# Performance work log

Measured on AMD Instinct MI355X. Metric: run time of the kernel, lower is better.

The kernel has to match this reference:

```python
import jax, jax.numpy as jnp
import numpy as np

VOCAB = 32000
HIDDEN = 1024
BATCH = 32
SEQ = 128


def setup_inputs() -> dict:
    key = jax.random.key(0)
    ks = jax.random.split(key, 8)
    p = lambda k, shape: (jax.random.normal(k, shape, dtype=jnp.float32) * 0.01)
    return {
        "x": jax.random.randint(ks[0], (BATCH, SEQ), 0, VOCAB, dtype=jnp.int64),
        "state": jnp.zeros((BATCH, HIDDEN), dtype=jnp.float32),
        "W_xr": p(ks[1], (VOCAB, HIDDEN)),
        "W_hr": p(ks[2], (HIDDEN, HIDDEN)),
        "b_r": jnp.zeros((HIDDEN,), dtype=jnp.float32),
        "W_xz": p(ks[3], (VOCAB, HIDDEN)),
        "W_hz": p(ks[4], (HIDDEN, HIDDEN)),
        "b_z": jnp.zeros((HIDDEN,), dtype=jnp.float32),
        "W_xh": p(ks[5], (VOCAB, HIDDEN)),
        "W_hh": p(ks[6], (HIDDEN, HIDDEN)),
        "b_h": jnp.zeros((HIDDEN,), dtype=jnp.float32),
        "W_ho": p(ks[7], (HIDDEN, VOCAB)),
        "b_o": jnp.zeros((VOCAB,), dtype=jnp.float32),
    }


def reference(x, state, W_xr, W_hr, b_r, W_xz, W_hz, b_z, W_xh, W_hh, b_h, W_ho, b_o):
    # x: (B, T) int tokens -> transpose to (T, B) like torch `x.T`.
    # one_hot(tok) @ W_x* is mathematically an embedding row gather: W_x*[tok].
    tokens = x.T  # (T, B)

    def step(h, tok):
        xr = W_xr[tok]  # (B, H)
        xz = W_xz[tok]
        xh = W_xh[tok]
        r = jax.nn.sigmoid(xr + h @ W_hr + b_r)
        z = jax.nn.sigmoid(xz + h @ W_hz + b_z)
        cand = jnp.tanh(xh + (r * h) @ W_hh + b_h)
        h_new = z * h + (1.0 - z) * cand
        out = h_new @ W_ho + b_o  # (B, V)
        return h_new, out

    final_state, outs = jax.lax.scan(step, state, tokens)  # outs: (T, B, V)
    # torch.cat(outputs, dim=0) concatenates per-step (B, V) blocks -> (T*B, V)
    return outs.reshape(-1, outs.shape[-1]), final_state
```

## Files before the change

kernel.cpp:

```cpp
#include <hip/hip_runtime.h>
#include <hip/hip_bf16.h>
#include <cstdint>
#include <cstddef>

#define VOCAB 32000
#define HIDDEN 1024
#define BATCH 32
#define SEQ 128

typedef __attribute__((ext_vector_type(8))) short short8v;
typedef __attribute__((ext_vector_type(4))) float float4v;
typedef __attribute__((ext_vector_type(2))) unsigned int uint2v;

__device__ __forceinline__ unsigned short f2bf(float f) {
    unsigned int x = __float_as_uint(f);
    unsigned int r = x + 0x7fffu + ((x >> 16) & 1u);
    return (unsigned short)(r >> 16);
}

__global__ __launch_bounds__(256) void k_transpose_bf(const float* __restrict__ in,
                                                      unsigned short* __restrict__ out,
                                                      int cols, int rows) {
    __shared__ float tile[64][65];
    const int jb = blockIdx.x;
    const int kb = blockIdx.y;
    const int t  = threadIdx.x;
    const int c  = t & 63;
    const int r0 = (t >> 6) * 16;
#pragma unroll
    for (int i = 0; i < 16; i++) {
        int r = r0 + i;
        tile[r][c] = in[(size_t)(kb * 64 + r) * cols + jb * 64 + c];
    }
    __syncthreads();
#pragma unroll
    for (int i = 0; i < 16; i++) {
        int r = r0 + i;
        out[(size_t)(jb * 64 + r) * rows + kb * 64 + c] = f2bf(tile[c][r]);
    }
}

__global__ __launch_bounds__(256) void k_init_hbf(const float* __restrict__ state,
                                                  unsigned short* __restrict__ hinit) {
    int i = blockIdx.x * 256 + threadIdx.x;
    if (i < BATCH * HIDDEN) hinit[i] = f2bf(state[i]);
}


#define WAIT_VM0 asm volatile("s_waitcnt vmcnt(0)" ::: "memory")
#define LGKM0    asm volatile("s_waitcnt lgkmcnt(0)" ::: "memory")

#define ST8_WT(P, V) \
    asm volatile("global_store_dwordx2 %0, %1, off sc0 sc1" ::"v"(P), "v"(V) : "memory")

__device__ __forceinline__ void row_poll(const unsigned int* row, unsigned int tag) {
    const unsigned int* p = row + (threadIdx.x & 63);
    int guard = 0;
    while (true) {
        unsigned int v = __hip_atomic_load(p, __ATOMIC_RELAXED, __HIP_MEMORY_SCOPE_AGENT);
        if (__all((int)(v >= tag))) break;
        if (++guard > 8192) break;
        __builtin_amdgcn_s_sleep(1);
    }
}

__global__ __launch_bounds__(64, 1) void k_rnn(const int* __restrict__ x,
                                               const float* __restrict__ state,
                                               const unsigned short* __restrict__ wrt,
                                               const unsigned short* __restrict__ wzt,
                                               const unsigned short* __restrict__ wht,
                                               const float* __restrict__ W_xr, const float* __restrict__ b_r,
                                               const float* __restrict__ W_xz, const float* __restrict__ b_z,
                                               const float* __restrict__ W_xh, const float* __restrict__ b_h,
                                               const unsigned short* __restrict__ hinit,
                                               unsigned short* __restrict__ hall,
                                               unsigned short* __restrict__ rhall,
                                               float* __restrict__ hstate_out,
                                               unsigned int* __restrict__ mbox) {
    const int bid = blockIdx.x;
    const int g   = bid >> 6;
    const int jsl = bid & 63;
    const int j0  = jsl * 16;
    const int b0  = g * 16;
    const int l   = threadIdx.x;
    const int llo = l & 15;
    const int lhi = l >> 4;
    const int jg  = j0 + llo;

    unsigned int* gm           = mbox + g * 64 * 64;
    const unsigned int* myrow  = gm + jsl * 64;
    unsigned int* pushtgt      = gm + l * 64 + jsl;

    __shared__ short8v wlds[3][32][64];
    __shared__ int xs[16 * SEQ];
    __shared__ unsigned short pack[16 * 16];

#pragma unroll
    for (int i = 0; i < 32; i++) {
        const size_t off = (size_t)jg * HIDDEN + i * 32 + lhi * 8;
        wlds[0][i][l] = *(const short8v*)&wrt[off];
        wlds[1][i][l] = *(const short8v*)&wzt[off];
        wlds[2][i][l] = *(const short8v*)&wht[off];
    }
    for (int i = l; i < 16 * SEQ; i += 64)
        xs[i] = x[(size_t)(b0 + (i >> 7)) * SEQ + (i & 127)];

    const float brv = b_r[jg], bzv = b_z[jg], bhv = b_h[jg];
    float4v hO;
#pragma unroll
    for (int q = 0; q < 4; q++) hO[q] = state[(b0 + 4 * lhi + q) * HIDDEN + jg];
    LGKM0;

    for (int t = 0; t < SEQ; t++) {
        const unsigned short* hprev =
            t ? (hall + (size_t)(t - 1) * BATCH * HIDDEN) : hinit;
        unsigned short* rhp = rhall + (size_t)t * BATCH * HIDDEN;
        unsigned short* hp  = hall + (size_t)t * BATCH * HIDDEN;

        int tok[4];
#pragma unroll
        for (int q = 0; q < 4; q++) tok[q] = xs[(4 * lhi + q) * SEQ + t];
        float xr[4], xz[4], xh[4];
#pragma unroll
        for (int q = 0; q < 4; q++) {
            xr[q] = W_xr[(size_t)tok[q] * HIDDEN + jg];
            xz[q] = W_xz[(size_t)tok[q] * HIDDEN + jg];
            xh[q] = W_xh[(size_t)tok[q] * HIDDEN + jg];
        }

        if (t) row_poll(myrow, 2u * (unsigned)t);

        short8v af[32];
#pragma unroll
        for (int i = 0; i < 32; i++)
            af[i] = *(const short8v*)&hprev[(b0 + llo) * HIDDEN + i * 32 + lhi * 8];

        float4v aR0 = {0.f, 0.f, 0.f, 0.f}, aR1 = {0.f, 0.f, 0.f, 0.f};
        float4v aZ0 = {0.f, 0.f, 0.f, 0.f}, aZ1 = {0.f, 0.f, 0.f, 0.f};
#pragma unroll
        for (int i = 0; i < 32; i += 2) {
            aR0 = __builtin_amdgcn_mfma_f32_16x16x32_bf16(af[i],     wlds[0][i][l],     aR0, 0, 0, 0);
            aZ0 = __builtin_amdgcn_mfma_f32_16x16x32_bf16(af[i],     wlds[1][i][l],     aZ0, 0, 0, 0);
            aR1 = __builtin_amdgcn_mfma_f32_16x16x32_bf16(af[i + 1], wlds[0][i + 1][l], aR1, 0, 0, 0);
            aZ1 = __builtin_amdgcn_mfma_f32_16x16x32_bf16(af[i + 1], wlds[1][i + 1][l], aZ1, 0, 0, 0);
        }

        float4v zv;
#pragma unroll
        for (int q = 0; q < 4; q++) {
            float sr = aR0[q] + aR1[q] + xr[q] + brv;
            float sz = aZ0[q] + aZ1[q] + xz[q] + bzv;
            float rv = 1.f / (1.f + __expf(-sr));
            zv[q]    = 1.f / (1.f + __expf(-sz));
            pack[(4 * lhi + q) * 16 + llo] = f2bf(rv * hO[q]);
        }
        LGKM0;
        __builtin_amdgcn_wave_barrier();
        {
            uint2v v = *(const uint2v*)&pack[(l >> 2) * 16 + (l & 3) * 4];
            ST8_WT(&rhp[(b0 + (l >> 2)) * HIDDEN + j0 + (l & 3) * 4], v);
            WAIT_VM0;
            __hip_atomic_store(pushtgt, 2u * (unsigned)t + 1u, __ATOMIC_RELAXED,
                               __HIP_MEMORY_SCOPE_AGENT);
        }

        row_poll(myrow, 2u * (unsigned)t + 1u);

        short8v ar[32];
#pragma unroll
        for (int i = 0; i < 32; i++)
            ar[i] = *(const short8v*)&rhp[(b0 + llo) * HIDDEN + i * 32 + lhi * 8];

        float4v aC0 = {0.f, 0.f, 0.f, 0.f}, aC1 = {0.f, 0.f, 0.f, 0.f};
#pragma unroll
        for (int i = 0; i < 32; i += 2) {
            aC0 = __builtin_amdgcn_mfma_f32_16x16x32_bf16(ar[i],     wlds[2][i][l],     aC0, 0, 0, 0);
            aC1 = __builtin_amdgcn_mfma_f32_16x16x32_bf16(ar[i + 1], wlds[2][i + 1][l], aC1, 0, 0, 0);
        }
#pragma unroll
        for (int q = 0; q < 4; q++) {
            float a = aC0[q] + aC1[q] + xh[q] + bhv;
            a = fminf(15.f, fmaxf(-15.f, a));
            float e2   = __expf(2.f * a);
            float cand = (e2 - 1.f) / (e2 + 1.f);
            float hn   = zv[q] * hO[q] + (1.f - zv[q]) * cand;
            hO[q]      = hn;
            pack[(4 * lhi + q) * 16 + llo] = f2bf(hn);
        }
        LGKM0;
        __builtin_amdgcn_wave_barrier();
        {
            uint2v v = *(const uint2v*)&pack[(l >> 2) * 16 + (l & 3) * 4];
            ST8_WT(&hp[(b0 + (l >> 2)) * HIDDEN + j0 + (l & 3) * 4], v);
            WAIT_VM0;
            __hip_atomic_store(pushtgt, 2u * (unsigned)t + 2u, __ATOMIC_RELAXED,
                               __HIP_MEMORY_SCOPE_AGENT);
        }
    }

#pragma unroll
    for (int q = 0; q < 4; q++)
        hstate_out[(b0 + 4 * lhi + q) * HIDDEN + jg] = hO[q];
}

#define BM 128
#define BN 128
#define BK 64

__device__ __forceinline__ void gload_lds16(const void* g, void* l) {
    __builtin_amdgcn_global_load_lds((const __attribute__((address_space(1))) void*)g,
                                     (__attribute__((address_space(3))) void*)l, 16, 0, 0);
}

__global__ __launch_bounds__(256, 2) void k_gemm(const unsigned short* __restrict__ A,
                                                 const unsigned short* __restrict__ B,
                                                 const float* __restrict__ bo,
                                                 float* __restrict__ out) {
    __shared__ unsigned short As[BM * BK];
    __shared__ unsigned short Bs[BN * BK];
    const int wg   = blockIdx.y * 250 + blockIdx.x;
    const int swz  = (wg & 7) * 1000 + (wg >> 3);
    const int nb   = swz % 250;
    const int mb   = swz / 250;
    const int tid  = threadIdx.x;
    const int lane = tid & 63;
    const int w    = tid >> 6;
    const int wm   = w >> 1, wn = w & 1;
    const int row0 = mb * BM, col0 = nb * BN;

    float4v acc[4][4];
#pragma unroll
    for (int i = 0; i < 4; i++)
#pragma unroll
        for (int j = 0; j < 4; j++) acc[i][j] = float4v{0.f, 0.f, 0.f, 0.f};

    for (int kt = 0; kt < HIDDEN / BK; kt++) {
#pragma unroll
        for (int i = 0; i < 4; i++) {
            int s   = i * 256 + tid;
            int row = s >> 3;
            int off = (s & 7) * 8;
            gload_lds16(A + (size_t)(row0 + row) * HIDDEN + kt * BK + off, &As[s * 8]);
            gload_lds16(B + (size_t)(col0 + row) * HIDDEN + kt * BK + off, &Bs[s * 8]);
        }
        __syncthreads();
#pragma unroll
        for (int kk = 0; kk < 2; kk++) {
            short8v af[4], bf[4];
#pragma unroll
            for (int i = 0; i < 4; i++) {
                int ar = wm * 64 + i * 16 + (lane & 15);
                af[i] = *(short8v*)&As[ar * BK + kk * 32 + (lane >> 4) * 8];
                int br = wn * 64 + i * 16 + (lane & 15);
                bf[i] = *(short8v*)&Bs[br * BK + kk * 32 + (lane >> 4) * 8];
            }
#pragma unroll
            for (int i = 0; i < 4; i++)
#pragma unroll
                for (int j = 0; j < 4; j++)
                    acc[i][j] = __builtin_amdgcn_mfma_f32_16x16x32_bf16(af[i], bf[j], acc[i][j], 0, 0, 0);
        }
        __syncthreads();
    }
#pragma unroll
    for (int i = 0; i < 4; i++) {
        int grow = row0 + wm * 64 + i * 16 + (lane >> 4) * 4;
#pragma unroll
        for (int j = 0; j < 4; j++) {
            int gcol   = col0 + wn * 64 + j * 16 + (lane & 15);
            float bias = bo[gcol];
#pragma unroll
            for (int r = 0; r < 4; r++) {
                out[(size_t)(grow + r) * VOCAB + gcol] = acc[i][j][r] + bias;
            }
        }
    }
}


extern "C" void kernel_launch(void* const* d_in, const int* in_sizes, int n_in,
                              void* d_out, int out_size, void* d_ws, size_t ws_size,
                              hipStream_t stream) {
    const int*   x     = (const int*)d_in[0];
    const float* state = (const float*)d_in[1];
    const float* W_xr  = (const float*)d_in[2];
    const float* W_hr  = (const float*)d_in[3];
    const float* b_r   = (const float*)d_in[4];
    const float* W_xz  = (const float*)d_in[5];
    const float* W_hz  = (const float*)d_in[6];
    const float* b_z   = (const float*)d_in[7];
    const float* W_xh  = (const float*)d_in[8];
    const float* W_hh  = (const float*)d_in[9];
    const float* b_h   = (const float*)d_in[10];
    const float* W_ho  = (const float*)d_in[11];
    const float* b_o   = (const float*)d_in[12];

    float* out    = (float*)d_out;
    float* hstate = out + (size_t)SEQ * BATCH * VOCAB;

    char* ws = (char*)d_ws;
    unsigned short* hall  = (unsigned short*)ws;
    unsigned short* rhall = (unsigned short*)(ws + 8388608);
    unsigned short* bt    = (unsigned short*)(ws + 16777216);
    unsigned short* wrt   = (unsigned short*)(ws + 82313216);
    unsigned short* wzt   = (unsigned short*)(ws + 84410368);
    unsigned short* wht   = (unsigned short*)(ws + 86507520);
    unsigned short* hinit = (unsigned short*)(ws + 88604672);
    unsigned int*   mbox  = (unsigned int*)(ws + 88670208);

    hipMemsetAsync(mbox, 0, 32768, stream);
    k_transpose_bf<<<dim3(16, 16), 256, 0, stream>>>(W_hr, wrt, HIDDEN, HIDDEN);
    k_transpose_bf<<<dim3(16, 16), 256, 0, stream>>>(W_hz, wzt, HIDDEN, HIDDEN);
    k_transpose_bf<<<dim3(16, 16), 256, 0, stream>>>(W_hh, wht, HIDDEN, HIDDEN);
    k_transpose_bf<<<dim3(500, 16), 256, 0, stream>>>(W_ho, bt, VOCAB, HIDDEN);
    k_init_hbf<<<128, 256, 0, stream>>>(state, hinit);

    k_rnn<<<128, 64, 0, stream>>>(x, state, wrt, wzt, wht, W_xr, b_r, W_xz, b_z, W_xh, b_h,
                                  hinit, hall, rhall, hstate, mbox);

    k_gemm<<<dim3(250, 32), 256, 0, stream>>>(hall, bt, b_o, out);
}
```

Before: 1.295 ms.

## Fuse recurrent kernel and output GEMM into one persistent kernel

Merges the sequential RNN kernel and the vocab-projection GEMM into a single launch. 128 blocks run the recurrence while 256 persistent blocks compute output tiles as soon as the matching timesteps are published, signalled by per-step done counters. This lets the large GEMM overlap with the latency-bound recurrence instead of waiting for it to finish. To fit the shared memory union, W_hh is no longer kept in LDS and is reloaded from global memory every step. The initial-state bf16 conversion kernel is also folded in, which adds risk from global-memory spin waits and from worker blocks sharing CUs with GEMM blocks.

Result: slower. 1.999 ms (+54.4%).

```diff
diff --git a/kernel.cpp b/kernel.cpp
--- a/kernel.cpp
+++ b/kernel.cpp
@@ -40,12 +40,6 @@
     }
 }
 
-__global__ __launch_bounds__(256) void k_init_hbf(const float* __restrict__ state,
-                                                  unsigned short* __restrict__ hinit) {
-    int i = blockIdx.x * 256 + threadIdx.x;
-    if (i < BATCH * HIDDEN) hinit[i] = f2bf(state[i]);
-}
-
 
 #define WAIT_VM0 asm volatile("s_waitcnt vmcnt(0)" ::: "memory")
 #define LGKM0    asm volatile("s_waitcnt lgkmcnt(0)" ::: "memory")
@@ -64,214 +58,258 @@
     }
 }
 
-__global__ __launch_bounds__(64, 1) void k_rnn(const int* __restrict__ x,
-                                               const float* __restrict__ state,
-                                               const unsigned short* __restrict__ wrt,
-                                               const unsigned short* __restrict__ wzt,
-                                               const unsigned short* __restrict__ wht,
-                                               const float* __restrict__ W_xr, const float* __restrict__ b_r,
-                                               const float* __restrict__ W_xz, const float* __restrict__ b_z,
-                                               const float* __restrict__ W_xh, const float* __restrict__ b_h,
-                                               const unsigned short* __restrict__ hinit,
-                                               unsigned short* __restrict__ hall,
-                                               unsigned short* __restrict__ rhall,
-                                               float* __restrict__ hstate_out,
-                                               unsigned int* __restrict__ mbox) {
-    const int bid = blockIdx.x;
-    const int g   = bid >> 6;
-    const int jsl = bid & 63;
-    const int j0  = jsl * 16;
-    const int b0  = g * 16;
-    const int l   = threadIdx.x;
-    const int llo = l & 15;
-    const int lhi = l >> 4;
-    const int jg  = j0 + llo;
-
-    unsigned int* gm           = mbox + g * 64 * 64;
-    const unsigned int* myrow  = gm + jsl * 64;
-    unsigned int* pushtgt      = gm + l * 64 + jsl;
-
-    __shared__ short8v wlds[3][32][64];
-    __shared__ int xs[16 * SEQ];
-    __shared__ unsigned short pack[16 * 16];
-
-#pragma unroll
-    for (int i = 0; i < 32; i++) {
-        const size_t off = (size_t)jg * HIDDEN + i * 32 + lhi * 8;
-        wlds[0][i][l] = *(const short8v*)&wrt[off];
-        wlds[1][i][l] = *(const short8v*)&wzt[off];
-        wlds[2][i][l] = *(const short8v*)&wht[off];
-    }
-    for (int i = l; i < 16 * SEQ; i += 64)
-        xs[i] = x[(size_t)(b0 + (i >> 7)) * SEQ + (i & 127)];
-
-    const float brv = b_r[jg], bzv = b_z[jg], bhv = b_h[jg];
-    float4v hO;
-#pragma unroll
-    for (int q = 0; q < 4; q++) hO[q] = state[(b0 + 4 * lhi + q) * HIDDEN + jg];
-    LGKM0;
-
-    for (int t = 0; t < SEQ; t++) {
-        const unsigned short* hprev =
-            t ? (hall + (size_t)(t - 1) * BATCH * HIDDEN) : hinit;
-        unsigned short* rhp = rhall + (size_t)t * BATCH * HIDDEN;
-        unsigned short* hp  = hall + (size_t)t * BATCH * HIDDEN;
-
-        int tok[4];
-#pragma unroll
-        for (int q = 0; q < 4; q++) tok[q] = xs[(4 * lhi + q) * SEQ + t];
-        float xr[4], xz[4], xh[4];
-#pragma unroll
-        for (int q = 0; q < 4; q++) {
-            xr[q] = W_xr[(size_t)tok[q] * HIDDEN + jg];
-            xz[q] = W_xz[(size_t)tok[q] * HIDDEN + jg];
-            xh[q] = W_xh[(size_t)tok[q] * HIDDEN + jg];
-        }
-
-        if (t) row_poll(myrow, 2u * (unsigned)t);
-
-        short8v af[32];
-#pragma unroll
-        for (int i = 0; i < 32; i++)
-            af[i] = *(const short8v*)&hprev[(b0 + llo) * HIDDEN + i * 32 + lhi * 8];
-
-        float4v aR0 = {0.f, 0.f, 0.f, 0.f}, aR1 = {0.f, 0.f, 0.f, 0.f};
-        float4v aZ0 = {0.f, 0.f, 0.f, 0.f}, aZ1 = {0.f, 0.f, 0.f, 0.f};
-#pragma unroll
-        for (int i = 0; i < 32; i += 2) {
-            aR0 = __builtin_amdgcn_mfma_f32_16x16x32_bf16(af[i],     wlds[0][i][l],     aR0, 0, 0, 0);
-            aZ0 = __builtin_amdgcn_mfma_f32_16x16x32_bf16(af[i],     wlds[1][i][l],     aZ0, 0, 0, 0);
-            aR1 = __builtin_amdgcn_mfma_f32_16x16x32_bf16(af[i + 1], wlds[0][i + 1][l], aR1, 0, 0, 0);
-            aZ1 = __builtin_amdgcn_mfma_f32_16x16x32_bf16(af[i + 1], wlds[1][i + 1][l], aZ1, 0, 0, 0);
-        }
-
-        float4v zv;
-#pragma unroll
-        for (int q = 0; q < 4; q++) {
-            float sr = aR0[q] + aR1[q] + xr[q] + brv;
-            float sz = aZ0[q] + aZ1[q] + xz[q] + bzv;
-            float rv = 1.f / (1.f + __expf(-sr));
-            zv[q]    = 1.f / (1.f + __expf(-sz));
-            pack[(4 * lhi + q) * 16 + llo] = f2bf(rv * hO[q]);
-        }
-        LGKM0;
-        __builtin_amdgcn_wave_barrier();
-        {
-            uint2v v = *(const uint2v*)&pack[(l >> 2) * 16 + (l & 3) * 4];
-            ST8_WT(&rhp[(b0 + (l >> 2)) * HIDDEN + j0 + (l & 3) * 4], v);
-            WAIT_VM0;
-            __hip_atomic_store(pushtgt, 2u * (unsigned)t + 1u, __ATOMIC_RELAXED,
-                               __HIP_MEMORY_SCOPE_AGENT);
-        }
-
-        row_poll(myrow, 2u * (unsigned)t + 1u);
-
-        short8v ar[32];
-#pragma unroll
-        for (int i = 0; i < 32; i++)
-            ar[i] = *(const short8v*)&rhp[(b0 + llo) * HIDDEN + i * 32 + lhi * 8];
-
-        float4v aC0 = {0.f, 0.f, 0.f, 0.f}, aC1 = {0.f, 0.f, 0.f, 0.f};
-#pragma unroll
-        for (int i = 0; i < 32; i += 2) {
-            aC0 = __builtin_amdgcn_mfma_f32_16x16x32_bf16(ar[i],     wlds[2][i][l],     aC0, 0, 0, 0);
-            aC1 = __builtin_amdgcn_mfma_f32_16x16x32_bf16(ar[i + 1], wlds[2][i + 1][l], aC1, 0, 0, 0);
-        }
-#pragma unroll
-        for (int q = 0; q < 4; q++) {
-            float a = aC0[q] + aC1[q] + xh[q] + bhv;
-            a = fminf(15.f, fmaxf(-15.f, a));
-            float e2   = __expf(2.f * a);
-            float cand = (e2 - 1.f) / (e2 + 1.f);
-            float hn   = zv[q] * hO[q] + (1.f - zv[q]) * cand;
-            hO[q]      = hn;
-            pack[(4 * lhi + q) * 16 + llo] = f2bf(hn);
-        }
-        LGKM0;
-        __builtin_amdgcn_wave_barrier();
-        {
-            uint2v v = *(const uint2v*)&pack[(l >> 2) * 16 + (l & 3) * 4];
-            ST8_WT(&hp[(b0 + (l >> 2)) * HIDDEN + j0 + (l & 3) * 4], v);
-            WAIT_VM0;
-            __hip_atomic_store(pushtgt, 2u * (unsigned)t + 2u, __ATOMIC_RELAXED,
-                               __HIP_MEMORY_SCOPE_AGENT);
-        }
-    }
-
-#pragma unroll
-    for (int q = 0; q < 4; q++)
-        hstate_out[(b0 + 4 * lhi + q) * HIDDEN + jg] = hO[q];
-}
-
-#define BM 128
-#define BN 128
-#define BK 64
-
 __device__ __forceinline__ void gload_lds16(const void* g, void* l) {
     __builtin_amdgcn_global_load_lds((const __attribute__((address_space(1))) void*)g,
                                      (__attribute__((address_space(3))) void*)l, 16, 0, 0);
 }
 
-__global__ __launch_bounds__(256, 2) void k_gemm(const unsigned short* __restrict__ A,
-                                                 const unsigned short* __restrict__ B,
-                                                 const float* __restrict__ bo,
-                                                 float* __restrict__ out) {
-    __shared__ unsigned short As[BM * BK];
-    __shared__ unsigned short Bs[BN * BK];
-    const int wg   = blockIdx.y * 250 + blockIdx.x;
-    const int swz  = (wg & 7) * 1000 + (wg >> 3);
-    const int nb   = swz % 250;
-    const int mb   = swz / 250;
+typedef struct {
+    short8v wlds[2][32][64];
+    unsigned short pack[16 * 16];
+} WorkerSM;
+typedef struct {
+    unsigned short As[128 * 64];
+    unsigned short Bs[128 * 64];
+    unsigned int ready;
+} GemmSM;
+
+__global__ __launch_bounds__(256, 1) void k_fused(const int* __restrict__ x,
+                                                  const float* __restrict__ state,
+                                                  const unsigned short* __restrict__ wrt,
+                                                  const unsigned short* __restrict__ wzt,
+                                                  const unsigned short* __restrict__ wht,
+                                                  const float* __restrict__ W_xr, const float* __restrict__ b_r,
+                                                  const float* __restrict__ W_xz, const float* __restrict__ b_z,
+                                                  const float* __restrict__ W_xh, const float* __restrict__ b_h,
+                                                  unsigned short* __restrict__ hall,
+                                                  unsigned short* __restrict__ rhall,
+                                                  float* __restrict__ hstate_out,
+                                                  unsigned int* __restrict__ mbox,
+                                                  unsigned int* __restrict__ done,
+                                                  const unsigned short* __restrict__ bt,
+                                                  const float* __restrict__ bo,
+                                                  float* __restrict__ out) {
+    __shared__ union { WorkerSM w; GemmSM g; } sm;
+    const int bid = blockIdx.x;
+
+    if (bid < 128) {
+        if (threadIdx.x >= 64) return;
+        const int g   = bid >> 6;
+        const int jsl = bid & 63;
+        const int j0  = jsl * 16;
+        const int b0  = g * 16;
+        const int l   = threadIdx.x;
+        const int llo = l & 15;
+        const int lhi = l >> 4;
+        const int jg  = j0 + llo;
+
+        unsigned int* gm          = mbox + g * 64 * 64;
+        const unsigned int* myrow = gm + jsl * 64;
+        unsigned int* pushtgt     = gm + l * 64 + jsl;
+
+#pragma unroll
+        for (int i = 0; i < 32; i++) {
+            const size_t off = (size_t)jg * HIDDEN + i * 32 + lhi * 8;
+            sm.w.wlds[0][i][l] = *(const short8v*)&wrt[off];
+            sm.w.wlds[1][i][l] = *(const short8v*)&wzt[off];
+        }
+        const float brv = b_r[jg], bzv = b_z[jg], bhv = b_h[jg];
+        float4v hO;
+#pragma unroll
+        for (int q = 0; q < 4; q++) hO[q] = state[(b0 + 4 * lhi + q) * HIDDEN + jg];
+        LGKM0;
+
+        for (int t = 0; t < SEQ; t++) {
+            unsigned short* rhp = rhall + (size_t)t * BATCH * HIDDEN;
+            unsigned short* hp  = hall + (size_t)t * BATCH * HIDDEN;
+
+            int tok[4];
+#pragma unroll
+            for (int q = 0; q < 4; q++) tok[q] = x[(size_t)(b0 + 4 * lhi + q) * SEQ + t];
+            float xr[4], xz[4], xh[4];
+#pragma unroll
+            for (int q = 0; q < 4; q++) {
+                xr[q] = W_xr[(size_t)tok[q] * HIDDEN + jg];
+                xz[q] = W_xz[(size_t)tok[q] * HIDDEN + jg];
+                xh[q] = W_xh[(size_t)tok[q] * HIDDEN + jg];
+            }
+
+            short8v af[32];
+            if (t == 0) {
+#pragma unroll
+                for (int i = 0; i < 32; i++) {
+                    const float* sp = &state[(size_t)(b0 + llo) * HIDDEN + i * 32 + lhi * 8];
+                    short8v v;
+#pragma unroll
+                    for (int e = 0; e < 8; e++) v[e] = (short)f2bf(sp[e]);
+                    af[i] = v;
+                }
+            } else {
+                row_poll(myrow, 2u * (unsigned)t);
+                const unsigned short* hprev = hall + (size_t)(t - 1) * BATCH * HIDDEN;
+#pragma unroll
+                for (int i = 0; i < 32; i++)
+                    af[i] = *(const short8v*)&hprev[(b0 + llo) * HIDDEN + i * 32 + lhi * 8];
+            }
+
+            float4v aR0 = {0.f, 0.f, 0.f, 0.f}, aR1 = {0.f, 0.f, 0.f, 0.f};
+            float4v aZ0 = {0.f, 0.f, 0.f, 0.f}, aZ1 = {0.f, 0.f, 0.f, 0.f};
+#pragma unroll
+            for (int i = 0; i < 32; i += 2) {
+                aR0 = __builtin_amdgcn_mfma_f32_16x16x32_bf16(af[i],     sm.w.wlds[0][i][l],     aR0, 0, 0, 0);
+                aZ0 = __builtin_amdgcn_mfma_f32_16x16x32_bf16(af[i],     sm.w.wlds[1][i][l],     aZ0, 0, 0, 0);
+                aR1 = __builtin_amdgcn_mfma_f32_16x16x32_bf16(af[i + 1], sm.w.wlds[0][i + 1][l], aR1, 0, 0, 0);
+                aZ1 = __builtin_amdgcn_mfma_f32_16x16x32_bf16(af[i + 1], sm.w.wlds[1][i + 1][l], aZ1, 0, 0, 0);
+            }
+
+            float4v zv;
+#pragma unroll
+            for (int q = 0; q < 4; q++) {
+                float sr = aR0[q] + aR1[q] + xr[q] + brv;
+                float sz = aZ0[q] + aZ1[q] + xz[q] + bzv;
+                float rv = 1.f / (1.f + __expf(-sr));
+                zv[q]    = 1.f / (1.f + __expf(-sz));
+                sm.w.pack[(4 * lhi + q) * 16 + llo] = f2bf(rv * hO[q]);
+            }
+            LGKM0;
+            __builtin_amdgcn_wave_barrier();
+            {
+                uint2v v = *(const uint2v*)&sm.w.pack[(l >> 2) * 16 + (l & 3) * 4];
+                ST8_WT(&rhp[(b0 + (l >> 2)) * HIDDEN + j0 + (l & 3) * 4], v);
+                WAIT_VM0;
+                __hip_atomic_store(pushtgt, 2u * (unsigned)t + 1u, __ATOMIC_RELAXED,
+                                   __HIP_MEMORY_SCOPE_AGENT);
+            }
+
+            short8v wh[32];
+#pragma unroll
+            for (int i = 0; i < 32; i++)
+                wh[i] = *(const short8v*)&wht[(size_t)jg * HIDDEN + i * 32 + lhi * 8];
+
+            row_poll(myrow, 2u * (unsigned)t + 1u);
+
+            short8v ar[32];
+#pragma unroll
+            for (int i = 0; i < 32; i++)
+                ar[i] = *(const short8v*)&rhp[(b0 + llo) * HIDDEN + i * 32 + lhi * 8];
+
+            float4v aC0 = {0.f, 0.f, 0.f, 0.f}, aC1 = {0.f, 0.f, 0.f, 0.f};
+#pragma unroll
+            for (int i = 0; i < 32; i += 2) {
+                aC0 = __builtin_amdgcn_mfma_f32_16x16x32_bf16(ar[i],     wh[i],     aC0, 0, 0, 0);
+                aC1 = __builtin_amdgcn_mfma_f32_16x16x32_bf16(ar[i + 1], wh[i + 1], aC1, 0, 0, 0);
+            }
+#pragma unroll
+            for (int q = 0; q < 4; q++) {
+                float a = aC0[q] + aC1[q] + xh[q] + bhv;
+                a = fminf(15.f, fmaxf(-15.f, a));
+                float e2   = __expf(2.f * a);
+                float cand = (e2 - 1.f) / (e2 + 1.f);
+                float hn   = zv[q] * hO[q] + (1.f - zv[q]) * cand;
+                hO[q]      = hn;
+                sm.w.pack[(4 * lhi + q) * 16 + llo] = f2bf(hn);
+            }
+            LGKM0;
+            __builtin_amdgcn_wave_barrier();
+            {
+                uint2v v = *(const uint2v*)&sm.w.pack[(l >> 2) * 16 + (l & 3) * 4];
+                ST8_WT(&hp[(b0 + (l >> 2)) * HIDDEN + j0 + (l & 3) * 4], v);
+                WAIT_VM0;
+                __hip_atomic_store(pushtgt, 2u * (unsigned)t + 2u, __ATOMIC_RELAXED,
+                                   __HIP_MEMORY_SCOPE_AGENT);
+                if (l == 0)
+                    __hip_atomic_fetch_add(&done[t], 1u, __ATOMIC_RELAXED,
+                                           __HIP_MEMORY_SCOPE_AGENT);
+            }
+        }
+
+#pragma unroll
+        for (int q = 0; q < 4; q++)
+            hstate_out[(b0 + 4 * lhi + q) * HIDDEN + jg] = hO[q];
+        return;
+    }
+
+    const int gbid = bid - 128;
     const int tid  = threadIdx.x;
+    if (tid == 0)
+        __hip_atomic_store(&sm.g.ready, 0u, __ATOMIC_RELAXED, __HIP_MEMORY_SCOPE_WORKGROUP);
+    __syncthreads();
+
     const int lane = tid & 63;
     const int w    = tid >> 6;
     const int wm   = w >> 1, wn = w & 1;
-    const int row0 = mb * BM, col0 = nb * BN;
-
-    float4v acc[4][4];
-#pragma unroll
-    for (int i = 0; i < 4; i++)
-#pragma unroll
-        for (int j = 0; j < 4; j++) acc[i][j] = float4v{0.f, 0.f, 0.f, 0.f};
-
-    for (int kt = 0; kt < HIDDEN / BK; kt++) {
+
+    for (int t8 = gbid; t8 < 8000; t8 += 256) {
+        const int mb = t8 / 250;
+        const int nb = t8 % 250;
+
+        {
+            int guard = 0;
+            while (true) {
+                unsigned int r = __hip_atomic_load(&sm.g.ready, __ATOMIC_RELAXED,
+                                                   __HIP_MEMORY_SCOPE_WORKGROUP);
+                if (r > (unsigned)mb) break;
+                if (tid == 0) {
+                    unsigned int d = __hip_atomic_load(&done[4 * mb + 3], __ATOMIC_RELAXED,
+                                                       __HIP_MEMORY_SCOPE_AGENT);
+                    if (d >= 128u)
+                        __hip_atomic_store(&sm.g.ready, (unsigned)(mb + 1), __ATOMIC_RELAXED,
+                                           __HIP_MEMORY_SCOPE_WORKGROUP);
+                    else
+                        __builtin_amdgcn_s_sleep(32);
+                } else {
+                    __builtin_amdgcn_s_sleep(8);
+                }
+                if (++guard > (1 << 18)) break;
+            }
+        }
+
+        const int row0 = mb * 128, col0 = nb * 128;
+        float4v acc[4][4];
+#pragma unroll
+        for (int i = 0; i < 4; i++)
+#pragma unroll
+            for (int j = 0; j < 4; j++) acc[i][j] = float4v{0.f, 0.f, 0.f, 0.f};
+
+        for (int kt = 0; kt < HIDDEN / 64; kt++) {
+#pragma unroll
+            for (int i = 0; i < 4; i++) {
+                int s   = i * 256 + tid;
+                int row = s >> 3;
+                int off = (s & 7) * 8;
+                gload_lds16(hall + (size_t)(row0 + row) * HIDDEN + kt * 64 + off, &sm.g.As[s * 8]);
+                gload_lds16(bt + (size_t)(col0 + row) * HIDDEN + kt * 64 + off, &sm.g.Bs[s * 8]);
+            }
+            __syncthreads();
+#pragma unroll
+            for (int kk = 0; kk < 2; kk++) {
+                short8v af[4], bf[4];
+#pragma unroll
+                for (int i = 0; i < 4; i++) {
+                    int ar = wm * 64 + i * 16 + (lane & 15);
+                    af[i] = *(short8v*)&sm.g.As[ar * 64 + kk * 32 + (lane >> 4) * 8];
+                    int br = wn * 64 + i * 16 + (lane & 15);
+                    bf[i] = *(short8v*)&sm.g.Bs[br * 64 + kk * 32 + (lane >> 4) * 8];
+                }
+#pragma unroll
+                for (int i = 0; i < 4; i++)
+#pragma unroll
+                    for (int j = 0; j < 4; j++)
+                        acc[i][j] = __builtin_amdgcn_mfma_f32_16x16x32_bf16(af[i], bf[j], acc[i][j], 0, 0, 0);
+            }
+            __syncthreads();
+        }
 #pragma unroll
         for (int i = 0; i < 4; i++) {
-            int s   = i * 256 + tid;
-            int row = s >> 3;
-            int off = (s & 7) * 8;
-            gload_lds16(A + (size_t)(row0 + row) * HIDDEN + kt * BK + off, &As[s * 8]);
-            gload_lds16(B + (size_t)(col0 + row) * HIDDEN + kt * BK + off, &Bs[s * 8]);
-        }
-        __syncthreads();
-#pragma unroll
-        for (int kk = 0; kk < 2; kk++) {
-            short8v af[4], bf[4];
-#pragma unroll
-            for (int i = 0; i < 4; i++) {
-                int ar = wm * 64 + i * 16 + (lane & 15);
-                af[i] = *(short8v*)&As[ar * BK + kk * 32 + (lane >> 4) * 8];
-                int br = wn * 64 + i * 16 + (lane & 15);
-                bf[i] = *(short8v*)&Bs[br * BK + kk * 32 + (lane >> 4) * 8];
-            }
-#pragma unroll
-            for (int i = 0; i < 4; i++)
-#pragma unroll
-                for (int j = 0; j < 4; j++)
-                    acc[i][j] = __builtin_amdgcn_mfma_f32_16x16x32_bf16(af[i], bf[j], acc[i][j], 0, 0, 0);
-        }
-        __syncthreads();
-    }
-#pragma unroll
-    for (int i = 0; i < 4; i++) {
-        int grow = row0 + wm * 64 + i * 16 + (lane >> 4) * 4;
-#pragma unroll
-        for (int j = 0; j < 4; j++) {
-            int gcol   = col0 + wn * 64 + j * 16 + (lane & 15);
-            float bias = bo[gcol];
-#pragma unroll
-            for (int r = 0; r < 4; r++) {
-                out[(size_t)(grow + r) * VOCAB + gcol] = acc[i][j][r] + bias;
+            int grow = row0 + wm * 64 + i * 16 + (lane >> 4) * 4;
+#pragma unroll
+            for (int j = 0; j < 4; j++) {
+                int gcol   = col0 + wn * 64 + j * 16 + (lane & 15);
+                float bias = bo[gcol];
+#pragma unroll
+                for (int r = 0; r < 4; r++) {
+                    out[(size_t)(grow + r) * VOCAB + gcol] = acc[i][j][r] + bias;
+                }
             }
         }
     }
@@ -305,18 +343,16 @@
     unsigned short* wrt   = (unsigned short*)(ws + 82313216);
     unsigned short* wzt   = (unsigned short*)(ws + 84410368);
     unsigned short* wht   = (unsigned short*)(ws + 86507520);
-    unsigned short* hinit = (unsigned short*)(ws + 88604672);
-    unsigned int*   mbox  = (unsigned int*)(ws + 88670208);
-
-    hipMemsetAsync(mbox, 0, 32768, stream);
+    unsigned int*   mbox  = (unsigned int*)(ws + 88604672);
+    unsigned int*   done  = (unsigned int*)(ws + 88637440);
+
+    hipMemsetAsync(mbox, 0, 32768 + 512, stream);
     k_transpose_bf<<<dim3(16, 16), 256, 0, stream>>>(W_hr, wrt, HIDDEN, HIDDEN);
     k_transpose_bf<<<dim3(16, 16), 256, 0, stream>>>(W_hz, wzt, HIDDEN, HIDDEN);
     k_transpose_bf<<<dim3(16, 16), 256, 0, stream>>>(W_hh, wht, HIDDEN, HIDDEN);
     k_transpose_bf<<<dim3(500, 16), 256, 0, stream>>>(W_ho, bt, VOCAB, HIDDEN);
-    k_init_hbf<<<128, 256, 0, stream>>>(state, hinit);
-
-    k_rnn<<<128, 64, 0, stream>>>(x, state, wrt, wzt, wht, W_xr, b_r, W_xz, b_z, W_xh, b_h,
-                                  hinit, hall, rhall, hstate, mbox);
-
-    k_gemm<<<dim3(250, 32), 256, 0, stream>>>(hall, bt, b_o, out);
-}
+
+    k_fused<<<384, 256, 0, stream>>>(x, state, wrt, wzt, wht, W_xr, b_r, W_xz, b_z,
+                                     W_xh, b_h, hall, rhall, hstate, mbox, done,
+                                     bt, b_o, out);
+}
```
